# Kernel optimization log

Measured on AMD Instinct MI355X. Metric: run time of the kernel, lower is better.

Reference implementation:

```python
import jax, jax.numpy as jnp
import numpy as np

B, N, M = 8, 4096, 77
Q_DIM, CTX_DIM = 1024, 768
H, D = 16, 64
INNER = H * D  # 1024


def setup_inputs() -> dict:
    key = jax.random.key(0)
    ks = jax.random.split(key, 7)
    x = jax.random.normal(ks[0], (B, N, Q_DIM), dtype=jnp.float32)
    context = jax.random.normal(ks[1], (B, M, CTX_DIM), dtype=jnp.float32)
    # Linear weights stored as [in, out] so y = x @ W (no bias for q/k/v).
    Wq = jax.random.normal(ks[2], (Q_DIM, INNER), dtype=jnp.float32) * (Q_DIM ** -0.5)
    Wk = jax.random.normal(ks[3], (CTX_DIM, INNER), dtype=jnp.float32) * (CTX_DIM ** -0.5)
    Wv = jax.random.normal(ks[4], (CTX_DIM, INNER), dtype=jnp.float32) * (CTX_DIM ** -0.5)
    Wo = jax.random.normal(ks[5], (INNER, Q_DIM), dtype=jnp.float32) * (INNER ** -0.5)
    bo = jax.random.normal(ks[6], (Q_DIM,), dtype=jnp.float32) * 0.01
    return {"x": x, "context": context, "Wq": Wq, "Wk": Wk, "Wv": Wv, "Wo": Wo, "bo": bo}


def reference(x, context, Wq, Wk, Wv, Wo, bo):
    scale = D ** -0.5
    # Project and split heads: [B, S, H*D] -> [B, H, S, D]
    def heads(t):
        b, s, _ = t.shape
        return t.reshape(b, s, H, D).transpose(0, 2, 1, 3)
    q = heads(x @ Wq)        # [B, H, N, D]
    k = heads(context @ Wk)  # [B, H, M, D]
    v = heads(context @ Wv)  # [B, H, M, D]
    scores = jnp.einsum('bhid,bhjd->bhij', q, k) * scale  # [B, H, N, M]
    attn = jax.nn.softmax(scores, axis=-1)
    out = jnp.einsum('bhij,bhjd->bhid', attn, v)          # [B, H, N, D]
    out = out.transpose(0, 2, 1, 3).reshape(x.shape[0], x.shape[1], INNER)
    return out @ Wo + bo  # dropout p=0.0 -> identity
```

## Files before the change

kernel.cpp:

```cpp
#include <hip/hip_runtime.h>
#include <hip/hip_bf16.h>

typedef _Float16 f16x8 __attribute__((ext_vector_type(8)));
typedef float f32x4 __attribute__((ext_vector_type(4)));

#define MFMA16(a, b, c) __builtin_amdgcn_mfma_f32_16x16x32_f16(a, b, c, 0, 0, 0)

__device__ __forceinline__ void load_lds16(const void* g, void* l) {
  __builtin_amdgcn_global_load_lds(
      (__attribute__((address_space(1))) void*)g,
      (__attribute__((address_space(3))) void*)l, 16, 0, 0);
}

__global__ __launch_bounds__(256) void k_cvt16(const float* __restrict__ in,
                                               _Float16* __restrict__ out, int n8) {
  int stride = gridDim.x * blockDim.x;
  for (int i = blockIdx.x * blockDim.x + threadIdx.x; i < n8; i += stride) {
    const float4* p = (const float4*)(in + (size_t)i * 8);
    float4 a = p[0], b = p[1];
    f16x8 v = {(_Float16)a.x, (_Float16)a.y, (_Float16)a.z, (_Float16)a.w,
               (_Float16)b.x, (_Float16)b.y, (_Float16)b.z, (_Float16)b.w};
    *(f16x8*)(out + (size_t)i * 8) = v;
  }
}

__global__ __launch_bounds__(256) void k_transpose(const float* __restrict__ in,
                                                   _Float16* __restrict__ out, int K, int N) {
  __shared__ float tile[64][65];
  int k0 = blockIdx.y * 64, n0 = blockIdx.x * 64;
  int t = threadIdx.x;
  {
    int nn = t & 63, kb = t >> 6;
#pragma unroll
    for (int i = 0; i < 16; ++i) {
      int kk = kb + i * 4;
      tile[kk][nn] = in[(size_t)(k0 + kk) * N + n0 + nn];
    }
  }
  __syncthreads();
  {
    int kk = t & 63, nb = t >> 6;
#pragma unroll
    for (int i = 0; i < 16; ++i) {
      int nn = nb + i * 4;
      out[(size_t)(n0 + nn) * K + k0 + kk] = (_Float16)tile[kk][nn];
    }
  }
}

__global__ __launch_bounds__(64) void k_kvproj(const _Float16* __restrict__ ctxh,
                                               const _Float16* __restrict__ Wkt,
                                               const _Float16* __restrict__ Wvt,
                                               _Float16* __restrict__ Kg,
                                               _Float16* __restrict__ Vtg) {
  int mt = blockIdx.x, nt = blockIdx.y;
  int lane = threadIdx.x;
  int l15 = lane & 15, lhi = lane >> 4;
  int arow = mt * 16 + l15;
  if (arow > 615) arow = 615;
  const _Float16* ap = ctxh + (size_t)arow * 768 + lhi * 8;
  const _Float16* kp = Wkt + (size_t)(nt * 16 + l15) * 768 + lhi * 8;
  const _Float16* vp = Wvt + (size_t)(nt * 16 + l15) * 768 + lhi * 8;
  f32x4 ak = {0.f, 0.f, 0.f, 0.f}, av = {0.f, 0.f, 0.f, 0.f};
#pragma unroll 4
  for (int ks = 0; ks < 24; ++ks) {
    f16x8 a = *(const f16x8*)(ap + ks * 32);
    f16x8 bk = *(const f16x8*)(kp + ks * 32);
    f16x8 bv = *(const f16x8*)(vp + ks * 32);
    ak = MFMA16(a, bk, ak);
    av = MFMA16(a, bv, av);
  }
  int n = nt * 16 + l15, h = n >> 6, d = n & 63;
#pragma unroll
  for (int j = 0; j < 4; ++j) {
    int gm = mt * 16 + lhi * 4 + j;
    if (gm < 616) {
      int b = gm / 77, m = gm - b * 77;
      Kg[((size_t)(b * 16 + h) * 77 + m) * 64 + d] = (_Float16)ak[j];
      Vtg[((size_t)(b * 16 + h) * 64 + d) * 128 + m] = (_Float16)av[j];
    }
  }
}

__global__ __launch_bounds__(256) void k_attn(const _Float16* __restrict__ Qh,
                                              const _Float16* __restrict__ Kg,
                                              const _Float16* __restrict__ Vtg,
                                              _Float16* __restrict__ Out) {
  __shared__ __align__(16) char Kl[80 * 128];
  __shared__ __align__(16) char Vl[64 * 256];
  __shared__ __align__(16) char Pl[4 * 16 * 256];
  int bh = blockIdx.y, b = bh >> 4, h = bh & 15;
  int t = threadIdx.x, wid = t >> 6, lane = t & 63;
  int l15 = lane & 15, lhi = lane >> 4;

  const _Float16* Kgp = Kg + (size_t)bh * (77 * 64);
  const _Float16* Vgp = Vtg + (size_t)bh * (64 * 128);

  for (int idx = t; idx < 640; idx += 256) {
    int m = idx >> 3, c = (idx & 7) * 8;
    f16x8 v = {};
    if (m < 77) v = *(const f16x8*)(Kgp + m * 64 + c);
    *(f16x8*)(Kl + ((m * 128 + c * 2) ^ ((m & 7) << 4))) = v;
  }
  for (int idx = t; idx < 1024; idx += 256) {
    int d = idx >> 4, c = (idx & 15) * 8;
    f16x8 v = *(const f16x8*)(Vgp + d * 128 + c);
    *(f16x8*)(Vl + ((d * 256 + c * 2) ^ ((d & 7) << 4))) = v;
  }
  char* myP = Pl + wid * 4096;
#pragma unroll
  for (int i = 0; i < 4; ++i) *(f16x8*)(myP + lane * 64 + i * 16) = f16x8{};
  __syncthreads();

  int qrow = b * 4096 + blockIdx.x * 64 + wid * 16 + l15;
  const _Float16* qp = Qh + (size_t)qrow * 1024 + h * 64 + lhi * 8;
  f16x8 q0 = *(const f16x8*)qp;
  f16x8 q1 = *(const f16x8*)(qp + 32);

  float e[5][4];
  float mx[4] = {-1e30f, -1e30f, -1e30f, -1e30f};
#pragma unroll
  for (int ct = 0; ct < 5; ++ct) {
    int m = ct * 16 + l15;
    int d0b = lhi * 16;
    f16x8 k0 = *(const f16x8*)(Kl + ((m * 128 + d0b) ^ ((m & 7) << 4)));
    f16x8 k1 = *(const f16x8*)(Kl + ((m * 128 + 64 + d0b) ^ ((m & 7) << 4)));
    f32x4 acc = {0.f, 0.f, 0.f, 0.f};
    acc = MFMA16(q0, k0, acc);
    acc = MFMA16(q1, k1, acc);
    bool valid = m < 77;
#pragma unroll
    for (int j = 0; j < 4; ++j) {
      float v = valid ? acc[j] * 0.125f : -1e30f;
      e[ct][j] = v;
      mx[j] = fmaxf(mx[j], v);
    }
  }
#pragma unroll
  for (int off = 1; off < 16; off <<= 1)
#pragma unroll
    for (int j = 0; j < 4; ++j) mx[j] = fmaxf(mx[j], __shfl_xor(mx[j], off, 64));
  float sm[4] = {0.f, 0.f, 0.f, 0.f};
#pragma unroll
  for (int ct = 0; ct < 5; ++ct)
#pragma unroll
    for (int j = 0; j < 4; ++j) {
      float ev = __expf(e[ct][j] - mx[j]);
      e[ct][j] = ev;
      sm[j] += ev;
    }
#pragma unroll
  for (int off = 1; off < 16; off <<= 1)
#pragma unroll
    for (int j = 0; j < 4; ++j) sm[j] += __shfl_xor(sm[j], off, 64);
  float rs[4];
#pragma unroll
  for (int j = 0; j < 4; ++j) rs[j] = 1.0f / sm[j];

#pragma unroll
  for (int ct = 0; ct < 5; ++ct) {
    int m = ct * 16 + l15;
#pragma unroll
    for (int j = 0; j < 4; ++j) {
      int r = lhi * 4 + j;
      *(_Float16*)(myP + ((r * 256 + m * 2) ^ ((r & 7) << 4))) =
          (_Float16)(e[ct][j] * rs[j]);
    }
  }

  f32x4 o[4] = {{0.f,0.f,0.f,0.f},{0.f,0.f,0.f,0.f},{0.f,0.f,0.f,0.f},{0.f,0.f,0.f,0.f}};
#pragma unroll
  for (int ks = 0; ks < 3; ++ks) {
    int m0b = ks * 64 + lhi * 16;
    f16x8 pa = *(const f16x8*)(myP + ((l15 * 256 + m0b) ^ ((l15 & 7) << 4)));
#pragma unroll
    for (int dt = 0; dt < 4; ++dt) {
      int d = dt * 16 + l15;
      f16x8 vb = *(const f16x8*)(Vl + ((d * 256 + m0b) ^ ((d & 7) << 4)));
      o[dt] = MFMA16(pa, vb, o[dt]);
    }
  }
  _Float16* op = Out + (size_t)(b * 4096 + blockIdx.x * 64 + wid * 16) * 1024 + h * 64;
#pragma unroll
  for (int dt = 0; dt < 4; ++dt)
#pragma unroll
    for (int j = 0; j < 4; ++j) {
      int r = lhi * 4 + j;
      op[(size_t)r * 1024 + dt * 16 + l15] = (_Float16)o[dt][j];
    }
}

template <int FINAL>
__global__ __launch_bounds__(512, 2) void k_gemm7(const _Float16* __restrict__ A,
                                                  const _Float16* __restrict__ Bt,
                                                  void* __restrict__ Cout,
                                                  const float* __restrict__ bias,
                                                  int M, int N, int K) {
  __shared__ __align__(16) char lds[131072];
  const int t = threadIdx.x, wid = t >> 6, lane = t & 63;
  const int wr = wid >> 2, wc = wid & 3;
  const int l15 = lane & 15, lhi = lane >> 4;

  int nwg = gridDim.x, bid = blockIdx.x;
  int wg = ((nwg & 7) == 0) ? ((bid & 7) * (nwg >> 3) + (bid >> 3)) : bid;
  const int nTN = N >> 8;
  const int tm = wg / nTN, tn = wg % nTN;

  const _Float16* Ag = A + (size_t)tm * 256 * K;
  const _Float16* Bg = Bt + (size_t)tn * 256 * K;
  const size_t stg = (size_t)(wid * 8 + (lane >> 3)) * K +
                     (size_t)(((lane & 7) ^ ((lane >> 3) & 7)) * 8);
  const int dstg = wid * 1024;

  const int x7 = l15 & 7;
  const int cs0 = (lhi ^ x7) << 4;
  const int cs1 = ((4 + lhi) ^ x7) << 4;
  const int aoff = wr * 16384 + l15 * 128;
  const int boff = 32768 + wc * 8192 + l15 * 128;

  f32x4 acc[8][4];
#pragma unroll
  for (int i = 0; i < 8; ++i)
#pragma unroll
    for (int j = 0; j < 4; ++j) acc[i][j] = f32x4{0.f, 0.f, 0.f, 0.f};
  f16x8 a0k0[4], a0k1[4], a1k0[4], a1k1[4];
  f16x8 b00[2], b01[2], b10[2], b11[2];

#define STG_A(T, RB) load_lds16(Ag + stg + (size_t)(RB) * K + (T) * 64, \
                                lds + ((T) & 1) * 65536 + (RB) * 128 + dstg)
#define STG_B(T, RB) load_lds16(Bg + stg + (size_t)(RB) * K + (T) * 64, \
                                lds + ((T) & 1) * 65536 + 32768 + (RB) * 128 + dstg)
#define STG_TILE(T) { STG_A(T, 0); STG_A(T, 64); STG_A(T, 128); STG_A(T, 192);  \
                      STG_B(T, 0); STG_B(T, 64); STG_B(T, 128); STG_B(T, 192); }
#define RDA(DST, BUF, MH, CS) { const int p_ = (BUF) * 65536 + aoff + (MH) * 8192; \
    _Pragma("unroll") for (int mf = 0; mf < 4; ++mf)                               \
      DST[mf] = *(const f16x8*)&lds[p_ + mf * 2048 + (CS)]; }
#define RDB(DST, BUF, NH, CS) { const int q_ = (BUF) * 65536 + boff + (NH) * 4096; \
    _Pragma("unroll") for (int nf = 0; nf < 2; ++nf)                               \
      DST[nf] = *(const f16x8*)&lds[q_ + nf * 2048 + (CS)]; }
#define MMC(MH, NH, AR, BR) { __builtin_amdgcn_s_setprio(1);                       \
    _Pragma("unroll") for (int mf = 0; mf < 4; ++mf)                               \
      _Pragma("unroll") for (int nf = 0; nf < 2; ++nf)                             \
        acc[(MH)*4+mf][(NH)*2+nf] = MFMA16(AR[mf], BR[nf],                         \
                                           acc[(MH)*4+mf][(NH)*2+nf]);             \
    __builtin_amdgcn_s_setprio(0); }
#define VM0 asm volatile("s_waitcnt vmcnt(0)" ::: "memory")
#define BAR __builtin_amdgcn_s_barrier()

#define TILE(BUF, T, STG_ON)                                                       \
  {                                                                                \
    VM0; BAR;                                                                      \
    RDA(a0k0, BUF, 0, cs0); RDB(b00, BUF, 0, cs0);                                 \
    RDB(b10, BUF, 1, cs0);                                                         \
    if (STG_ON) STG_TILE((T) + 1);                                                 \
    MMC(0, 0, a0k0, b00);                                                          \
    RDA(a1k0, BUF, 1, cs0); MMC(0, 1, a0k0, b10);                                  \
    RDA(a1k1, BUF, 1, cs1); MMC(1, 1, a1k0, b10);                                  \
    RDB(b01, BUF, 0, cs1);  MMC(1, 0, a1k0, b00);                                  \
    RDB(b11, BUF, 1, cs1);  MMC(1, 0, a1k1, b01);                                  \
    RDA(a0k1, BUF, 0, cs1); MMC(1, 1, a1k1, b11);                                  \
    MMC(0, 1, a0k1, b11);                                                          \
    MMC(0, 0, a0k1, b01);                                                          \
  }

  const int nT = K >> 6;

  STG_TILE(0);

  for (int i = 0; i < (nT >> 1) - 1; ++i) {
    TILE(0, 2 * i, true);
    TILE(1, 2 * i + 1, true);
  }
  TILE(0, nT - 2, true);
  TILE(1, nT - 1, false);

  const long rbase = (long)tm * 256 + wr * 128;
  const int cbase = tn * 256 + wc * 64;
#pragma unroll
  for (int mf = 0; mf < 8; ++mf)
#pragma unroll
    for (int nf = 0; nf < 4; ++nf) {
      int c = cbase + nf * 16 + l15;
      float bv = FINAL ? bias[c] : 0.f;
#pragma unroll
      for (int j = 0; j < 4; ++j) {
        long r = rbase + mf * 16 + lhi * 4 + j;
        float v = acc[mf][nf][j];
        if (FINAL) ((float*)Cout)[r * N + c] = v + bv;
        else ((_Float16*)Cout)[r * N + c] = (_Float16)v;
      }
    }
#undef STG_A
#undef STG_B
#undef STG_TILE
#undef RDA
#undef RDB
#undef MMC
#undef TILE
#undef VM0
#undef BAR
}

extern "C" void kernel_launch(void* const* d_in, const int* in_sizes, int n_in,
                              void* d_out, int out_size, void* d_ws, size_t ws_size,
                              hipStream_t stream) {
  const float* x   = (const float*)d_in[0];
  const float* ctx = (const float*)d_in[1];
  const float* Wq  = (const float*)d_in[2];
  const float* Wk  = (const float*)d_in[3];
  const float* Wv  = (const float*)d_in[4];
  const float* Wo  = (const float*)d_in[5];
  const float* bo  = (const float*)d_in[6];

  char* ws = (char*)d_ws;
  _Float16* xh   = (_Float16*)(ws + 0);
  _Float16* Wqt  = (_Float16*)(ws + 67108864);
  _Float16* Wkt  = (_Float16*)(ws + 69206016);
  _Float16* Wvt  = (_Float16*)(ws + 70778880);
  _Float16* Wot  = (_Float16*)(ws + 72351744);
  _Float16* ctxh = (_Float16*)(ws + 74448896);
  _Float16* Kg   = (_Float16*)(ws + 75395072);
  _Float16* Vtg  = (_Float16*)(ws + 76656640);
  _Float16* Qh   = (_Float16*)d_out;

  k_cvt16<<<4096, 256, 0, stream>>>(x, xh, 33554432 / 8);
  k_cvt16<<<231, 256, 0, stream>>>(ctx, ctxh, 473088 / 8);
  k_transpose<<<dim3(16, 16), 256, 0, stream>>>(Wq, Wqt, 1024, 1024);
  k_transpose<<<dim3(16, 12), 256, 0, stream>>>(Wk, Wkt, 768, 1024);
  k_transpose<<<dim3(16, 12), 256, 0, stream>>>(Wv, Wvt, 768, 1024);
  k_transpose<<<dim3(16, 16), 256, 0, stream>>>(Wo, Wot, 1024, 1024);
  hipMemsetAsync(Vtg, 0, 2097152, stream);
  k_kvproj<<<dim3(39, 64), 64, 0, stream>>>(ctxh, Wkt, Wvt, Kg, Vtg);
  k_gemm7<0><<<dim3(512), dim3(512), 0, stream>>>(xh, Wqt, (void*)Qh, nullptr, 32768, 1024, 1024);
  k_attn<<<dim3(64, 128), 256, 0, stream>>>(Qh, Kg, Vtg, xh);
  k_gemm7<1><<<dim3(512), dim3(512), 0, stream>>>(xh, Wot, d_out, bo, 32768, 1024, 1024);
}
```

Before: 284.6 us.

## Switch GEMM to 32x32x16 MFMA tiles and fuse preprocessing launches into one kernel

The GEMM inner loop moves from 16x16x32 MFMA fragments to 32x32x16 fragments. Each wave now holds 4x2 32x32 accumulators and reads k-chunks in four swizzled passes, which means fewer LDS reads per FLOP and fewer MFMA issues. Separately, the fp16 conversions of x and context, the four weight transposes and the Vtg memset are merged into a single block-dispatched prep kernel, removing several launches. The cost is a different register and LDS access pattern in the GEMM and a new epilogue row mapping that must match the 32x32 MFMA output layout.

```diff
diff --git a/kernel.cpp b/kernel.cpp
--- a/kernel.cpp
+++ b/kernel.cpp
@@ -3,8 +3,10 @@
 
 typedef _Float16 f16x8 __attribute__((ext_vector_type(8)));
 typedef float f32x4 __attribute__((ext_vector_type(4)));
+typedef float f32x16 __attribute__((ext_vector_type(16)));
 
 #define MFMA16(a, b, c) __builtin_amdgcn_mfma_f32_16x16x32_f16(a, b, c, 0, 0, 0)
+#define MFMA32(a, b, c) __builtin_amdgcn_mfma_f32_32x32x16_f16(a, b, c, 0, 0, 0)
 
 __device__ __forceinline__ void load_lds16(const void* g, void* l) {
   __builtin_amdgcn_global_load_lds(
@@ -12,38 +14,69 @@
       (__attribute__((address_space(3))) void*)l, 16, 0, 0);
 }
 
-__global__ __launch_bounds__(256) void k_cvt16(const float* __restrict__ in,
-                                               _Float16* __restrict__ out, int n8) {
-  int stride = gridDim.x * blockDim.x;
-  for (int i = blockIdx.x * blockDim.x + threadIdx.x; i < n8; i += stride) {
-    const float4* p = (const float4*)(in + (size_t)i * 8);
-    float4 a = p[0], b = p[1];
+__global__ __launch_bounds__(256) void k_prep(const float* __restrict__ x,
+                                              const float* __restrict__ ctx,
+                                              const float* __restrict__ Wq,
+                                              const float* __restrict__ Wk,
+                                              const float* __restrict__ Wv,
+                                              const float* __restrict__ Wo,
+                                              _Float16* __restrict__ xh,
+                                              _Float16* __restrict__ ctxh,
+                                              _Float16* __restrict__ Wqt,
+                                              _Float16* __restrict__ Wkt,
+                                              _Float16* __restrict__ Wvt,
+                                              _Float16* __restrict__ Wot,
+                                              _Float16* __restrict__ Vtg) {
+  __shared__ float tile[64][65];
+  const int b = blockIdx.x, t = threadIdx.x;
+
+  if (b < 4096) {
+    for (int i = b * 256 + t; i < 4194304; i += 4096 * 256) {
+      const float4* p = (const float4*)(x + (size_t)i * 8);
+      float4 a = p[0], c = p[1];
+      f16x8 v = {(_Float16)a.x, (_Float16)a.y, (_Float16)a.z, (_Float16)a.w,
+                 (_Float16)c.x, (_Float16)c.y, (_Float16)c.z, (_Float16)c.w};
+      *(f16x8*)(xh + (size_t)i * 8) = v;
+    }
+    return;
+  }
+  if (b < 4327) {
+    int i = (b - 4096) * 256 + t;
+    const float4* p = (const float4*)(ctx + (size_t)i * 8);
+    float4 a = p[0], c = p[1];
     f16x8 v = {(_Float16)a.x, (_Float16)a.y, (_Float16)a.z, (_Float16)a.w,
-               (_Float16)b.x, (_Float16)b.y, (_Float16)b.z, (_Float16)b.w};
-    *(f16x8*)(out + (size_t)i * 8) = v;
-  }
-}
-
-__global__ __launch_bounds__(256) void k_transpose(const float* __restrict__ in,
-                                                   _Float16* __restrict__ out, int K, int N) {
-  __shared__ float tile[64][65];
-  int k0 = blockIdx.y * 64, n0 = blockIdx.x * 64;
-  int t = threadIdx.x;
+               (_Float16)c.x, (_Float16)c.y, (_Float16)c.z, (_Float16)c.w};
+    *(f16x8*)(ctxh + (size_t)i * 8) = v;
+    return;
+  }
+  if (b >= 5223) {
+    int i = (b - 5223) * 256 + t;
+    ((f16x8*)Vtg)[i] = f16x8{};
+    return;
+  }
+  const float* tin;
+  _Float16* tout;
+  int TK, TN, i;
+  if (b < 4583)      { tin = Wq; tout = Wqt; TK = 1024; TN = 1024; i = b - 4327; }
+  else if (b < 4775) { tin = Wk; tout = Wkt; TK = 768;  TN = 1024; i = b - 4583; }
+  else if (b < 4967) { tin = Wv; tout = Wvt; TK = 768;  TN = 1024; i = b - 4775; }
+  else               { tin = Wo; tout = Wot; TK = 1024; TN = 1024; i = b - 4967; }
+  int n0 = (i & 15) * 64, k0 = (i >> 4) * 64;
   {
     int nn = t & 63, kb = t >> 6;
 #pragma unroll
-    for (int i = 0; i < 16; ++i) {
-      int kk = kb + i * 4;
-      tile[kk][nn] = in[(size_t)(k0 + kk) * N + n0 + nn];
+    for (int s = 0; s < 16; ++s) {
+      int kk = kb + s * 4;
+      tile[kk][nn] = tin[(size_t)(k0 + kk) * TN + n0 + nn];
     }
   }
   __syncthreads();
   {
     int kk = t & 63, nb = t >> 6;
 #pragma unroll
-    for (int i = 0; i < 16; ++i) {
-      int nn = nb + i * 4;
-      out[(size_t)(n0 + nn) * K + k0 + kk] = (_Float16)tile[kk][nn];
+    for (int s = 0; s < 16; ++s) {
+      int nn = nb + s * 4;
+      tout[(size_t)(n0 + nn) * TK + k0 + kk] = (_Float16)tile[kk][nn];
     }
   }
 }
@@ -191,7 +224,7 @@
 }
 
 template <int FINAL>
-__global__ __launch_bounds__(512, 2) void k_gemm7(const _Float16* __restrict__ A,
+__global__ __launch_bounds__(512, 2) void k_gemm8(const _Float16* __restrict__ A,
                                                   const _Float16* __restrict__ Bt,
                                                   void* __restrict__ Cout,
                                                   const float* __restrict__ bias,
@@ -199,7 +232,7 @@
   __shared__ __align__(16) char lds[131072];
   const int t = threadIdx.x, wid = t >> 6, lane = t & 63;
   const int wr = wid >> 2, wc = wid & 3;
-  const int l15 = lane & 15, lhi = lane >> 4;
+  const int l31 = lane & 31, hi = lane >> 5;
 
   int nwg = gridDim.x, bid = blockIdx.x;
   int wg = ((nwg & 7) == 0) ? ((bid & 7) * (nwg >> 3) + (bid >> 3)) : bid;
@@ -212,19 +245,19 @@
                      (size_t)(((lane & 7) ^ ((lane >> 3) & 7)) * 8);
   const int dstg = wid * 1024;
 
-  const int x7 = l15 & 7;
-  const int cs0 = (lhi ^ x7) << 4;
-  const int cs1 = ((4 + lhi) ^ x7) << 4;
-  const int aoff = wr * 16384 + l15 * 128;
-  const int boff = 32768 + wc * 8192 + l15 * 128;
-
-  f32x4 acc[8][4];
-#pragma unroll
-  for (int i = 0; i < 8; ++i)
-#pragma unroll
-    for (int j = 0; j < 4; ++j) acc[i][j] = f32x4{0.f, 0.f, 0.f, 0.f};
-  f16x8 a0k0[4], a0k1[4], a1k0[4], a1k1[4];
-  f16x8 b00[2], b01[2], b10[2], b11[2];
+  const int x7 = l31 & 7;
+  const int cka = ((0 + hi) ^ x7) << 4;
+  const int ckb = ((2 + hi) ^ x7) << 4;
+  const int ckc = ((4 + hi) ^ x7) << 4;
+  const int ckd = ((6 + hi) ^ x7) << 4;
+  const int abase = (wr * 128 + l31) * 128;
+  const int bbase = 32768 + (wc * 64 + l31) * 128;
+
+  f32x16 acc[4][2];
+#pragma unroll
+  for (int i = 0; i < 4; ++i) { acc[i][0] = f32x16{}; acc[i][1] = f32x16{}; }
+  f16x8 xa0, xa1, xa2, xa3, xb0, xb1;
+  f16x8 ya0, ya1, ya2, ya3, yb0, yb1;
 
 #define STG_A(T, RB) load_lds16(Ag + stg + (size_t)(RB) * K + (T) * 64, \
                                 lds + ((T) & 1) * 65536 + (RB) * 128 + dstg)
@@ -232,35 +265,36 @@
                                 lds + ((T) & 1) * 65536 + 32768 + (RB) * 128 + dstg)
 #define STG_TILE(T) { STG_A(T, 0); STG_A(T, 64); STG_A(T, 128); STG_A(T, 192);  \
                       STG_B(T, 0); STG_B(T, 64); STG_B(T, 128); STG_B(T, 192); }
-#define RDA(DST, BUF, MH, CS) { const int p_ = (BUF) * 65536 + aoff + (MH) * 8192; \
-    _Pragma("unroll") for (int mf = 0; mf < 4; ++mf)                               \
-      DST[mf] = *(const f16x8*)&lds[p_ + mf * 2048 + (CS)]; }
-#define RDB(DST, BUF, NH, CS) { const int q_ = (BUF) * 65536 + boff + (NH) * 4096; \
-    _Pragma("unroll") for (int nf = 0; nf < 2; ++nf)                               \
-      DST[nf] = *(const f16x8*)&lds[q_ + nf * 2048 + (CS)]; }
-#define MMC(MH, NH, AR, BR) { __builtin_amdgcn_s_setprio(1);                       \
-    _Pragma("unroll") for (int mf = 0; mf < 4; ++mf)                               \
-      _Pragma("unroll") for (int nf = 0; nf < 2; ++nf)                             \
-        acc[(MH)*4+mf][(NH)*2+nf] = MFMA16(AR[mf], BR[nf],                         \
-                                           acc[(MH)*4+mf][(NH)*2+nf]);             \
+#define RDK(A0, A1, A2, A3, B0, B1, BUF, CK) {                                  \
+    const int pa_ = (BUF) * 65536 + abase + (CK);                               \
+    A0 = *(const f16x8*)&lds[pa_];                                              \
+    A1 = *(const f16x8*)&lds[pa_ + 4096];                                       \
+    A2 = *(const f16x8*)&lds[pa_ + 8192];                                       \
+    A3 = *(const f16x8*)&lds[pa_ + 12288];                                      \
+    const int pb_ = (BUF) * 65536 + bbase + (CK);                               \
+    B0 = *(const f16x8*)&lds[pb_];                                              \
+    B1 = *(const f16x8*)&lds[pb_ + 4096]; }
+#define MMK(A0, A1, A2, A3, B0, B1) { __builtin_amdgcn_s_setprio(1);            \
+    acc[0][0] = MFMA32(A0, B0, acc[0][0]); acc[0][1] = MFMA32(A0, B1, acc[0][1]); \
+    acc[1][0] = MFMA32(A1, B0, acc[1][0]); acc[1][1] = MFMA32(A1, B1, acc[1][1]); \
+    acc[2][0] = MFMA32(A2, B0, acc[2][0]); acc[2][1] = MFMA32(A2, B1, acc[2][1]); \
+    acc[3][0] = MFMA32(A3, B0, acc[3][0]); acc[3][1] = MFMA32(A3, B1, acc[3][1]); \
     __builtin_amdgcn_s_setprio(0); }
 #define VM0 asm volatile("s_waitcnt vmcnt(0)" ::: "memory")
 #define BAR __builtin_amdgcn_s_barrier()
 
-#define TILE(BUF, T, STG_ON)                                                       \
-  {                                                                                \
-    VM0; BAR;                                                                      \
-    RDA(a0k0, BUF, 0, cs0); RDB(b00, BUF, 0, cs0);                                 \
-    RDB(b10, BUF, 1, cs0);                                                         \
-    if (STG_ON) STG_TILE((T) + 1);                                                 \
-    MMC(0, 0, a0k0, b00);                                                          \
-    RDA(a1k0, BUF, 1, cs0); MMC(0, 1, a0k0, b10);                                  \
-    RDA(a1k1, BUF, 1, cs1); MMC(1, 1, a1k0, b10);                                  \
-    RDB(b01, BUF, 0, cs1);  MMC(1, 0, a1k0, b00);                                  \
-    RDB(b11, BUF, 1, cs1);  MMC(1, 0, a1k1, b01);                                  \
-    RDA(a0k1, BUF, 0, cs1); MMC(1, 1, a1k1, b11);                                  \
-    MMC(0, 1, a0k1, b11);                                                          \
-    MMC(0, 0, a0k1, b01);                                                          \
+#define TILE(BUF, T, STG_ON)                                                    \
+  {                                                                             \
+    VM0; BAR;                                                                   \
+    RDK(xa0, xa1, xa2, xa3, xb0, xb1, BUF, cka);                                \
+    if (STG_ON) STG_TILE((T) + 1);                                              \
+    RDK(ya0, ya1, ya2, ya3, yb0, yb1, BUF, ckb);                                \
+    MMK(xa0, xa1, xa2, xa3, xb0, xb1);                                          \
+    RDK(xa0, xa1, xa2, xa3, xb0, xb1, BUF, ckc);                                \
+    MMK(ya0, ya1, ya2, ya3, yb0, yb1);                                          \
+    RDK(ya0, ya1, ya2, ya3, yb0, yb1, BUF, ckd);                                \
+    MMK(xa0, xa1, xa2, xa3, xb0, xb1);                                          \
+    MMK(ya0, ya1, ya2, ya3, yb0, yb1);                                          \
   }
 
   const int nT = K >> 6;
@@ -277,15 +311,15 @@
   const long rbase = (long)tm * 256 + wr * 128;
   const int cbase = tn * 256 + wc * 64;
 #pragma unroll
-  for (int mf = 0; mf < 8; ++mf)
-#pragma unroll
-    for (int nf = 0; nf < 4; ++nf) {
-      int c = cbase + nf * 16 + l15;
+  for (int mf = 0; mf < 4; ++mf)
+#pragma unroll
+    for (int nf = 0; nf < 2; ++nf) {
+      int c = cbase + nf * 32 + l31;
       float bv = FINAL ? bias[c] : 0.f;
 #pragma unroll
-      for (int j = 0; j < 4; ++j) {
-        long r = rbase + mf * 16 + lhi * 4 + j;
-        float v = acc[mf][nf][j];
+      for (int reg = 0; reg < 16; ++reg) {
+        long r = rbase + mf * 32 + (reg & 3) + ((reg >> 2) << 3) + (hi << 2);
+        float v = acc[mf][nf][reg];
         if (FINAL) ((float*)Cout)[r * N + c] = v + bv;
         else ((_Float16*)Cout)[r * N + c] = (_Float16)v;
       }
@@ -293,9 +327,8 @@
 #undef STG_A
 #undef STG_B
 #undef STG_TILE
-#undef RDA
-#undef RDB
-#undef MMC
+#undef RDK
+#undef MMK
 #undef TILE
 #undef VM0
 #undef BAR
@@ -323,15 +356,10 @@
   _Float16* Vtg  = (_Float16*)(ws + 76656640);
   _Float16* Qh   = (_Float16*)d_out;
 
-  k_cvt16<<<4096, 256, 0, stream>>>(x, xh, 33554432 / 8);
-  k_cvt16<<<231, 256, 0, stream>>>(ctx, ctxh, 473088 / 8);
-  k_transpose<<<dim3(16, 16), 256, 0, stream>>>(Wq, Wqt, 1024, 1024);
-  k_transpose<<<dim3(16, 12), 256, 0, stream>>>(Wk, Wkt, 768, 1024);
-  k_transpose<<<dim3(16, 12), 256, 0, stream>>>(Wv, Wvt, 768, 1024);
-  k_transpose<<<dim3(16, 16), 256, 0, stream>>>(Wo, Wot, 1024, 1024);
-  hipMemsetAsync(Vtg, 0, 2097152, stream);
+  k_prep<<<5735, 256, 0, stream>>>(x, ctx, Wq, Wk, Wv, Wo,
+                                   xh, ctxh, Wqt, Wkt, Wvt, Wot, Vtg);
   k_kvproj<<<dim3(39, 64), 64, 0, stream>>>(ctxh, Wkt, Wvt, Kg, Vtg);
-  k_gemm7<0><<<dim3(512), dim3(512), 0, stream>>>(xh, Wqt, (void*)Qh, nullptr, 32768, 1024, 1024);
+  k_gemm8<0><<<dim3(512), dim3(512), 0, stream>>>(xh, Wqt, (void*)Qh, nullptr, 32768, 1024, 1024);
   k_attn<<<dim3(64, 128), 256, 0, stream>>>(Qh, Kg, Vtg, xh);
-  k_gemm7<1><<<dim3(512), dim3(512), 0, stream>>>(xh, Wot, d_out, bo, 32768, 1024, 1024);
-}
+  k_gemm8<1><<<dim3(512), dim3(512), 0, stream>>>(xh, Wot, d_out, bo, 32768, 1024, 1024);
+}
```

Measured after the change: 279.1 us. No clear change (-1.9%).
